# Performance work log

Measured on AMD Instinct MI355X. Metric: run time of the kernel, lower is better.

## Reference

```python
import jax, jax.numpy as jnp
import numpy as np

B, S, I, H, O, L = 16, 2048, 128, 512, 128, 2

def setup_inputs() -> dict:
    key = jax.random.key(0)
    ks = jax.random.split(key, 20)
    sI = 1.0 / np.sqrt(I)
    sH = 1.0 / np.sqrt(H)
    inp = {
        "x": jax.random.normal(ks[0], (B, S, I), jnp.float32),
        "hidden_state": jax.random.normal(ks[1], (B, L, H), jnp.float32),
        # layer 0 (input dim I)
        "Wxz0": jax.random.normal(ks[2], (H, I), jnp.float32) * sI,
        "Whz0": jax.random.normal(ks[3], (H, H), jnp.float32) * sH,
        "bhz0": jax.random.normal(ks[4], (H,), jnp.float32) * sH,
        "Wxr0": jax.random.normal(ks[5], (H, I), jnp.float32) * sI,
        "Whr0": jax.random.normal(ks[6], (H, H), jnp.float32) * sH,
        "bhr0": jax.random.normal(ks[7], (H,), jnp.float32) * sH,
        # layer 1 (input dim H)
        "Wxz1": jax.random.normal(ks[8], (H, H), jnp.float32) * sH,
        "Whz1": jax.random.normal(ks[9], (H, H), jnp.float32) * sH,
        "bhz1": jax.random.normal(ks[10], (H,), jnp.float32) * sH,
        "Wxr1": jax.random.normal(ks[11], (H, H), jnp.float32) * sH,
        "Whr1": jax.random.normal(ks[12], (H, H), jnp.float32) * sH,
        "bhr1": jax.random.normal(ks[13], (H,), jnp.float32) * sH,
        # output head
        "Why": jax.random.normal(ks[14], (O, H), jnp.float32) * sH,
        "by": jax.random.normal(ks[15], (O,), jnp.float32) * sH,
    }
    return inp


def _gru_layer(xs, h0, Wxz, Whz, bhz, Wxr, Whr, bhr):
    # Precompute input projections in one batched GEMM: [B,S,H]
    xz = jnp.einsum('bsi,hi->bsh', xs, Wxz)
    xr = jnp.einsum('bsi,hi->bsh', xs, Wxr)

    def step(h, inp):
        xz_t, xr_t = inp  # [B,H] each
        z = jax.nn.sigmoid(xz_t + h @ Whz.T + bhz)
        r = jax.nn.sigmoid(xr_t + h @ Whr.T + bhr)
        # NOTE: faithful to source bug: gt reuses fc_xr / fc_hr (with bias)
        g = jnp.tanh(xr_t + (r * h) @ Whr.T + bhr)
        hn = z * h + (1.0 - z) * g
        return hn, hn

    hT, ys = jax.lax.scan(step, h0, (jnp.swapaxes(xz, 0, 1), jnp.swapaxes(xr, 0, 1)))
    return jnp.swapaxes(ys, 0, 1), hT  # [B,S,H], [B,H]


def reference(x, hidden_state, Wxz0, Whz0, bhz0, Wxr0, Whr0, bhr0,
              Wxz1, Whz1, bhz1, Wxr1, Whr1, bhr1, Why, by):
    y0, h0T = _gru_layer(x, hidden_state[:, 0, :], Wxz0, Whz0, bhz0, Wxr0, Whr0, bhr0)
    y1, h1T = _gru_layer(y0, hidden_state[:, 1, :], Wxz1, Whz1, bhz1, Wxr1, Whr1, bhr1)
    out = jnp.einsum('bsh,oh->bso', y1, Why) + by  # [B,S,O]
    h_final = jnp.stack([h0T, h1T], axis=1)  # [B,L,H]
    return out, h_final
```

## Files before the change

kernel.cpp:

```cpp
#include <hip/hip_runtime.h>
#include <stdint.h>

#define Bv 16
#define Sv 2048
#define Iv 128
#define Hv 512
#define Ov 128
#define RP 520

typedef __bf16 v8bf __attribute__((ext_vector_type(8)));
typedef float v4f __attribute__((ext_vector_type(4)));
#define MFMA(a, b, c) __builtin_amdgcn_mfma_f32_16x16x32_bf16((a), (b), (c), 0, 0, 0)

__device__ __forceinline__ float sigf(float x) { return 1.0f / (1.0f + __expf(-x)); }
__device__ __forceinline__ float tanh_fast(float x) { return 2.0f / (1.0f + __expf(-2.0f * x)) - 1.0f; }

__device__ __forceinline__ unsigned f2bf(float f) {
  union { __bf16 h; unsigned short u; } c; c.h = (__bf16)f; return (unsigned)c.u;
}
__device__ __forceinline__ float bf2f(unsigned short u) {
  union { __bf16 h; unsigned short u; } c; c.u = u; return (float)c.h;
}

__device__ __forceinline__ v8bf cvt8(const float* p) {
  v8bf r;
#pragma unroll
  for (int i = 0; i < 8; i++) r[i] = (__bf16)p[i];
  return r;
}

__device__ __forceinline__ uint64_t ld64(const uint64_t* p) {
  return __hip_atomic_load((uint64_t*)p, __ATOMIC_RELAXED, __HIP_MEMORY_SCOPE_AGENT);
}
__device__ __forceinline__ void st32(unsigned* p, unsigned v) {
  __hip_atomic_store(p, v, __ATOMIC_RELAXED, __HIP_MEMORY_SCOPE_AGENT);
}
__device__ __forceinline__ unsigned ld32(const unsigned* p) {
  return __hip_atomic_load((unsigned*)p, __ATOMIC_RELAXED, __HIP_MEMORY_SCOPE_AGENT);
}

__device__ __forceinline__ void store_slice(unsigned* dslot, int rb, int j0, int rj, float val) {
  unsigned bits = f2bf(val);
  unsigned nb = (unsigned)__shfl_xor((int)bits, 1);
  if ((rj & 1) == 0)
    st32(dslot + rb * 256 + ((j0 + rj) >> 1), bits | (nb << 16));
}

__device__ __forceinline__ void poll1(const unsigned* s, unsigned want, int tid) {
  unsigned r = 0;
  for (;;) {
    unsigned v = ld32(s + (tid & 31));
    if (__all(v == want) || ++r > (1u << 20)) break;
  }
}
__device__ __forceinline__ void poll2(const unsigned* sA, unsigned wA,
                                      const unsigned* sB, unsigned wB, int tid) {
  unsigned r = 0;
  for (;;) {
    unsigned a = ld32(sA + (tid & 31));
    unsigned b = ld32(sB + (tid & 31));
    if (__all((a == wA) && (b == wB)) || ++r > (1u << 20)) break;
  }
}

__device__ __forceinline__ void read_stage(const unsigned* dslot, unsigned short* lds, int tid) {
  const uint64_t* p = (const uint64_t*)dslot;
  uint64_t w[8];
#pragma unroll
  for (int i = 0; i < 8; i++) w[i] = ld64(p + i * 256 + tid);
#pragma unroll
  for (int i = 0; i < 8; i++) {
    int d = i * 256 + tid;
    *(uint64_t*)(lds + (d >> 7) * RP + (d & 127) * 4) = w[i];
  }
}
__device__ __forceinline__ void read_stage2(const unsigned* dA, unsigned short* lA,
                                            const unsigned* dB, unsigned short* lB, int tid) {
  const uint64_t* pA = (const uint64_t*)dA;
  const uint64_t* pB = (const uint64_t*)dB;
  uint64_t wa[8], wb[8];
#pragma unroll
  for (int i = 0; i < 8; i++) wa[i] = ld64(pA + i * 256 + tid);
#pragma unroll
  for (int i = 0; i < 8; i++) wb[i] = ld64(pB + i * 256 + tid);
#pragma unroll
  for (int i = 0; i < 8; i++) {
    int d = i * 256 + tid;
    *(uint64_t*)(lA + (d >> 7) * RP + (d & 127) * 4) = wa[i];
    *(uint64_t*)(lB + (d >> 7) * RP + (d & 127) * 4) = wb[i];
  }
}

__global__ __launch_bounds__(256, 1) void gru_fused(
    const float* __restrict__ x, const float* __restrict__ hs,
    const float* __restrict__ Wxz0, const float* __restrict__ Whz0, const float* __restrict__ bhz0,
    const float* __restrict__ Wxr0, const float* __restrict__ Whr0, const float* __restrict__ bhr0,
    const float* __restrict__ Wxz1, const float* __restrict__ Whz1, const float* __restrict__ bhz1,
    const float* __restrict__ Wxr1, const float* __restrict__ Whr1, const float* __restrict__ bhr1,
    const float* __restrict__ Why, const float* __restrict__ by,
    float* __restrict__ out, char* __restrict__ ws, int D) {
  const int tid = threadIdx.x;
  const int wave = tid >> 6;
  const int lane = tid & 63;
  const int lm = lane & 15;
  const int lq = lane >> 4;
  const int rb = tid >> 4;
  const int rj = tid & 15;
  const int m0 = D - 1;

  unsigned* prog = (unsigned*)ws;
  unsigned* h0s = (unsigned*)(ws + 1024);
  unsigned* h1s = h0s + D * 32;
  unsigned* u0s = h1s + 128;
  unsigned* u1s = u0s + 64;
  unsigned* h0d = (unsigned*)(ws + 16384);
  unsigned* h1d = h0d + (size_t)D * 4096;
  unsigned* u0d = h1d + 4 * 4096;
  unsigned* u1d = u0d + 2 * 4096;

  __shared__ unsigned short stA[16 * RP];
  __shared__ unsigned short stB[16 * RP];
  __shared__ unsigned short stC[16 * RP];
  __shared__ float red[4][4][16][17];

  const bool L0 = (blockIdx.x < 32);
  const int wg = L0 ? blockIdx.x : (blockIdx.x - 32);
  const int j0 = wg << 4;
  const bool OW = (!L0) && (wg < 8);
  const int jrow = j0 + lm;

  {
    float h0v = hs[((size_t)rb * 2 + (L0 ? 0 : 1)) * Hv + j0 + rj];
    store_slice(L0 ? h0d : h1d, rb, j0, rj, h0v);
    __syncthreads();
    if (tid == 0) st32((L0 ? h0s : h1s) + wg, 1u);
  }

  if (L0) {
    v8bf wzx0 = cvt8(Wxz0 + (size_t)jrow * Iv + wave * 32 + lq * 8);
    v8bf wrx0 = cvt8(Wxr0 + (size_t)jrow * Iv + wave * 32 + lq * 8);
    v8bf wzh[4], wrh[4];
#pragma unroll
    for (int kb = 0; kb < 4; kb++) {
      int k = wave * 128 + kb * 32 + lq * 8;
      wzh[kb] = cvt8(Whz0 + (size_t)jrow * Hv + k);
      wrh[kb] = cvt8(Whr0 + (size_t)jrow * Hv + k);
    }
    float bz = bhz0[j0 + rj], br = bhr0[j0 + rj];

    const int xk = wave * 32 + lq * 8;
    float4 xp0 = *(const float4*)(x + ((size_t)lm * Sv + 0) * Iv + xk);
    float4 xp1 = *(const float4*)(x + ((size_t)lm * Sv + 0) * Iv + xk + 4);

    for (int t = 0; t < Sv; ++t) {
      if (t >= D - 1 && tid < 32) {
        unsigned need = (unsigned)(t - D + 2), it = 0;
        while (ld32(prog + tid) < need)
          if (++it > (1u << 20)) break;
      }
      poll1(h0s + (t & m0) * 32, (unsigned)(t + 1), tid);
      read_stage(h0d + (size_t)(t & m0) * 4096, stA, tid);
      __syncthreads();
      float hval = bf2f(stA[rb * RP + j0 + rj]);
      const unsigned short* hrow = stA + lm * RP;
      v8bf ah[4];
#pragma unroll
      for (int kb = 0; kb < 4; kb++)
        ah[kb] = *(const v8bf*)(hrow + wave * 128 + kb * 32 + lq * 8);
      v8bf ax;
      {
        float xf[8] = {xp0.x, xp0.y, xp0.z, xp0.w, xp1.x, xp1.y, xp1.z, xp1.w};
#pragma unroll
        for (int i = 0; i < 8; i++) ax[i] = (__bf16)xf[i];
      }
      v4f az = {0, 0, 0, 0}, axr = {0, 0, 0, 0}, ahr = {0, 0, 0, 0};
      az = MFMA(ax, wzx0, az);
      axr = MFMA(ax, wrx0, axr);
#pragma unroll
      for (int kb = 0; kb < 4; kb++) {
        az = MFMA(ah[kb], wzh[kb], az);
        ahr = MFMA(ah[kb], wrh[kb], ahr);
      }
#pragma unroll
      for (int v = 0; v < 4; v++) {
        red[0][wave][lq * 4 + v][lm] = az[v];
        red[1][wave][lq * 4 + v][lm] = axr[v];
        red[2][wave][lq * 4 + v][lm] = ahr[v];
      }
      __syncthreads();
      float zs = 0, xrs = 0, hrs = 0;
#pragma unroll
      for (int w = 0; w < 4; w++) {
        zs += red[0][w][rb][rj];
        xrs += red[1][w][rb][rj];
        hrs += red[2][w][rb][rj];
      }
      float z = sigf(zs + bz);
      float r = sigf(xrs + hrs + br);
      store_slice(u0d + (t & 1) * 4096, rb, j0, rj, r * hval);
      if (t + 1 < Sv) {
        xp0 = *(const float4*)(x + ((size_t)lm * Sv + (t + 1)) * Iv + xk);
        xp1 = *(const float4*)(x + ((size_t)lm * Sv + (t + 1)) * Iv + xk + 4);
      }
      __syncthreads();
      if (tid == 0) st32(u0s + (t & 1) * 32 + wg, (unsigned)(t + 1));
      poll1(u0s + (t & 1) * 32, (unsigned)(t + 1), tid);
      read_stage(u0d + (size_t)(t & 1) * 4096, stB, tid);
      __syncthreads();
      const unsigned short* urow = stB + lm * RP;
      v4f ag = {0, 0, 0, 0};
#pragma unroll
      for (int kb = 0; kb < 4; kb++) {
        v8bf au = *(const v8bf*)(urow + wave * 128 + kb * 32 + lq * 8);
        ag = MFMA(au, wrh[kb], ag);
      }
#pragma unroll
      for (int v = 0; v < 4; v++) red[3][wave][lq * 4 + v][lm] = ag[v];
      __syncthreads();
      float gs = 0;
#pragma unroll
      for (int w = 0; w < 4; w++) gs += red[3][w][rb][rj];
      float g = tanh_fast(xrs + gs + br);
      float hn = z * hval + (1.f - z) * g;
      store_slice(h0d + (size_t)((t + 1) & m0) * 4096, rb, j0, rj, hn);
      if (t == Sv - 1) out[(size_t)Bv * Sv * Ov + ((size_t)rb * 2 + 0) * Hv + j0 + rj] = hn;
      __syncthreads();
      if (tid == 0) st32(h0s + ((t + 1) & m0) * 32 + wg, (unsigned)(t + 2));
    }
  } else {
    v8bf wzx1[4], wrx1[4], wzh[4], wrh[4], wo[4];
#pragma unroll
    for (int kb = 0; kb < 4; kb++) {
      int k = wave * 128 + kb * 32 + lq * 8;
      wzx1[kb] = cvt8(Wxz1 + (size_t)jrow * Hv + k);
      wrx1[kb] = cvt8(Wxr1 + (size_t)jrow * Hv + k);
      wzh[kb] = cvt8(Whz1 + (size_t)jrow * Hv + k);
      wrh[kb] = cvt8(Whr1 + (size_t)jrow * Hv + k);
      if (OW) wo[kb] = cvt8(Why + (size_t)jrow * Hv + k);
    }
    float bz = bhz1[j0 + rj], br = bhr1[j0 + rj];
    float bo = OW ? by[j0 + rj] : 0.f;

    for (int t = 0; t < Sv; ++t) {
      poll2(h0s + ((t + 1) & m0) * 32, (unsigned)(t + 2),
            h1s + (t & 3) * 32, (unsigned)(t + 1), tid);
      read_stage2(h0d + (size_t)((t + 1) & m0) * 4096, stA,
                  h1d + (size_t)(t & 3) * 4096, stB, tid);
      __syncthreads();
      if (tid == 0) st32(prog + wg, (unsigned)(t + 1));
      float hval = bf2f(stB[rb * RP + j0 + rj]);
      const unsigned short* yrow = stA + lm * RP;
      const unsigned short* hrow = stB + lm * RP;
      v4f az = {0, 0, 0, 0}, axr = {0, 0, 0, 0}, ahr = {0, 0, 0, 0}, ao = {0, 0, 0, 0};
      v8bf ahf[4];
#pragma unroll
      for (int kb = 0; kb < 4; kb++) {
        int k = wave * 128 + kb * 32 + lq * 8;
        v8bf ay = *(const v8bf*)(yrow + k);
        ahf[kb] = *(const v8bf*)(hrow + k);
        az = MFMA(ay, wzx1[kb], az);
        az = MFMA(ahf[kb], wzh[kb], az);
        axr = MFMA(ay, wrx1[kb], axr);
        ahr = MFMA(ahf[kb], wrh[kb], ahr);
      }
      if (OW && t > 0) {
#pragma unroll
        for (int kb = 0; kb < 4; kb++) ao = MFMA(ahf[kb], wo[kb], ao);
      }
#pragma unroll
      for (int v = 0; v < 4; v++) {
        red[0][wave][lq * 4 + v][lm] = az[v];
        red[1][wave][lq * 4 + v][lm] = axr[v];
        red[2][wave][lq * 4 + v][lm] = ahr[v];
        red[3][wave][lq * 4 + v][lm] = ao[v];
      }
      __syncthreads();
      float zs = 0, xrs = 0, hrs = 0, os = 0;
#pragma unroll
      for (int w = 0; w < 4; w++) {
        zs += red[0][w][rb][rj];
        xrs += red[1][w][rb][rj];
        hrs += red[2][w][rb][rj];
        os += red[3][w][rb][rj];
      }
      float z = sigf(zs + bz);
      float r = sigf(xrs + hrs + br);
      store_slice(u1d + (t & 1) * 4096, rb, j0, rj, r * hval);
      if (OW && t > 0) out[((size_t)rb * Sv + (t - 1)) * Ov + j0 + rj] = os + bo;
      __syncthreads();
      if (tid == 0) st32(u1s + (t & 1) * 32 + wg, (unsigned)(t + 1));
      poll1(u1s + (t & 1) * 32, (unsigned)(t + 1), tid);
      read_stage(u1d + (size_t)(t & 1) * 4096, stC, tid);
      __syncthreads();
      const unsigned short* urow = stC + lm * RP;
      v4f ag = {0, 0, 0, 0};
#pragma unroll
      for (int kb = 0; kb < 4; kb++) {
        v8bf au = *(const v8bf*)(urow + wave * 128 + kb * 32 + lq * 8);
        ag = MFMA(au, wrh[kb], ag);
      }
#pragma unroll
      for (int v = 0; v < 4; v++) red[3][wave][lq * 4 + v][lm] = ag[v];
      __syncthreads();
      float gs = 0;
#pragma unroll
      for (int w = 0; w < 4; w++) gs += red[3][w][rb][rj];
      float g = tanh_fast(xrs + gs + br);
      float hn = z * hval + (1.f - z) * g;
      store_slice(h1d + (size_t)((t + 1) & 3) * 4096, rb, j0, rj, hn);
      if (t == Sv - 1) out[(size_t)Bv * Sv * Ov + ((size_t)rb * 2 + 1) * Hv + j0 + rj] = hn;
      __syncthreads();
      if (tid == 0) st32(h1s + ((t + 1) & 3) * 32 + wg, (unsigned)(t + 2));
    }
    if (OW) {
      poll1(h1s + (Sv & 3) * 32, (unsigned)(Sv + 1), tid);
      read_stage(h1d + (size_t)(Sv & 3) * 4096, stB, tid);
      __syncthreads();
      const unsigned short* hrow = stB + lm * RP;
      v4f ao = {0, 0, 0, 0};
#pragma unroll
      for (int kb = 0; kb < 4; kb++) {
        v8bf ah = *(const v8bf*)(hrow + wave * 128 + kb * 32 + lq * 8);
        ao = MFMA(ah, wo[kb], ao);
      }
#pragma unroll
      for (int v = 0; v < 4; v++) red[3][wave][lq * 4 + v][lm] = ao[v];
      __syncthreads();
      float os = 0;
#pragma unroll
      for (int w = 0; w < 4; w++) os += red[3][w][rb][rj];
      out[((size_t)rb * Sv + (Sv - 1)) * Ov + j0 + rj] = os + bo;
    }
  }
}

extern "C" void kernel_launch(void* const* d_in, const int* in_sizes, int n_in,
                              void* d_out, int out_size, void* d_ws, size_t ws_size,
                              hipStream_t stream) {
  const float* x = (const float*)d_in[0];
  const float* hs = (const float*)d_in[1];
  const float* Wxz0 = (const float*)d_in[2];
  const float* Whz0 = (const float*)d_in[3];
  const float* bhz0 = (const float*)d_in[4];
  const float* Wxr0 = (const float*)d_in[5];
  const float* Whr0 = (const float*)d_in[6];
  const float* bhr0 = (const float*)d_in[7];
  const float* Wxz1 = (const float*)d_in[8];
  const float* Whz1 = (const float*)d_in[9];
  const float* bhz1 = (const float*)d_in[10];
  const float* Wxr1 = (const float*)d_in[11];
  const float* Whr1 = (const float*)d_in[12];
  const float* bhr1 = (const float*)d_in[13];
  const float* Why = (const float*)d_in[14];
  const float* by = (const float*)d_in[15];
  float* out = (float*)d_out;

  int D = 64;
  while (D > 4 && 16384 + (size_t)(D + 8) * 16384 > ws_size) D >>= 1;

  hipMemsetAsync(d_ws, 0, 4096, stream);
  hipLaunchKernelGGL(gru_fused, dim3(64), dim3(256), 0, stream,
                     x, hs, Wxz0, Whz0, bhz0, Wxr0, Whr0, bhr0,
                     Wxz1, Whz1, bhz1, Wxr1, Whr1, bhr1, Why, by,
                     out, (char*)d_ws, D);
}
```

Measured before the change: 9.004 ms.

## Replace flag-based cross-block sync with tagged per-element data and fragment-layout polling

Each bf16 hidden-state element is now stored in a 32-bit word together with a timestep tag. Data sits in a permuted layout matching the MFMA fragment order, so each lane polls and loads its own operands straight from global memory. This removes the separate flag arrays, the LDS staging buffers, the __syncthreads around stores and the flag publish/poll round trip, trading one fence-like handshake per stage for doubled workspace traffic and per-lane validation loops. It also moves the prefetch and progress wait earlier, adds a separate reduction slot for the g-gate, and memsets the whole workspace each call.

Result: slower. 25.53 ms (+183.5%).

```diff
diff --git a/kernel.cpp b/kernel.cpp
--- a/kernel.cpp
+++ b/kernel.cpp
@@ -6,7 +6,6 @@
 #define Iv 128
 #define Hv 512
 #define Ov 128
-#define RP 520
 
 typedef __bf16 v8bf __attribute__((ext_vector_type(8)));
 typedef float v4f __attribute__((ext_vector_type(4)));
@@ -39,55 +38,79 @@
   return __hip_atomic_load((unsigned*)p, __ATOMIC_RELAXED, __HIP_MEMORY_SCOPE_AGENT);
 }
 
-__device__ __forceinline__ void store_slice(unsigned* dslot, int rb, int j0, int rj, float val) {
-  unsigned bits = f2bf(val);
-  unsigned nb = (unsigned)__shfl_xor((int)bits, 1);
-  if ((rj & 1) == 0)
-    st32(dslot + rb * 256 + ((j0 + rj) >> 1), bits | (nb << 16));
-}
-
-__device__ __forceinline__ void poll1(const unsigned* s, unsigned want, int tid) {
+__device__ __forceinline__ int pidx(int b, int c) {
+  return ((c >> 7) << 11) | (((c >> 3) & 3) << 9) | (b << 5) | (((c >> 5) & 3) << 3) | (c & 7);
+}
+
+__device__ __forceinline__ void pollfrag(const unsigned* slot, int wl, unsigned tag, uint64_t* W) {
+  const uint64_t* p = (const uint64_t*)slot + wl;
+  const uint64_t want = ((uint64_t)tag << 16) | ((uint64_t)tag << 48);
+  const uint64_t MSK = 0xffff0000ffff0000ull;
   unsigned r = 0;
   for (;;) {
-    unsigned v = ld32(s + (tid & 31));
-    if (__all(v == want) || ++r > (1u << 20)) break;
+    uint64_t a0 = ld64(p), a1 = ld64(p + 4), a2 = ld64(p + 8), a3 = ld64(p + 12);
+    bool probe = ((a0 & MSK) == want) && ((a1 & MSK) == want) &&
+                 ((a2 & MSK) == want) && ((a3 & MSK) == want);
+    if (__all(probe)) {
+#pragma unroll
+      for (int i = 0; i < 16; i++) W[i] = ld64(p + i);
+      bool ok = true;
+#pragma unroll
+      for (int i = 0; i < 16; i++) ok &= ((W[i] & MSK) == want);
+      if (__all(ok)) return;
+    }
+    if (++r > (1u << 20)) {
+#pragma unroll
+      for (int i = 0; i < 16; i++) W[i] = ld64(p + i);
+      return;
+    }
   }
 }
-__device__ __forceinline__ void poll2(const unsigned* sA, unsigned wA,
-                                      const unsigned* sB, unsigned wB, int tid) {
+
+__device__ __forceinline__ void pollfrag2(const unsigned* sA, unsigned tA,
+                                          const unsigned* sB, unsigned tB,
+                                          int wl, uint64_t* WA, uint64_t* WB) {
+  const uint64_t* pA = (const uint64_t*)sA + wl;
+  const uint64_t* pB = (const uint64_t*)sB + wl;
+  const uint64_t wantA = ((uint64_t)tA << 16) | ((uint64_t)tA << 48);
+  const uint64_t wantB = ((uint64_t)tB << 16) | ((uint64_t)tB << 48);
+  const uint64_t MSK = 0xffff0000ffff0000ull;
   unsigned r = 0;
   for (;;) {
-    unsigned a = ld32(sA + (tid & 31));
-    unsigned b = ld32(sB + (tid & 31));
-    if (__all((a == wA) && (b == wB)) || ++r > (1u << 20)) break;
+    uint64_t a0 = ld64(pA), a1 = ld64(pA + 4), a2 = ld64(pA + 8), a3 = ld64(pA + 12);
+    uint64_t b0 = ld64(pB), b1 = ld64(pB + 4), b2 = ld64(pB + 8), b3 = ld64(pB + 12);
+    bool probe = ((a0 & MSK) == wantA) && ((a1 & MSK) == wantA) &&
+                 ((a2 & MSK) == wantA) && ((a3 & MSK) == wantA) &&
+                 ((b0 & MSK) == wantB) && ((b1 & MSK) == wantB) &&
+                 ((b2 & MSK) == wantB) && ((b3 & MSK) == wantB);
+    if (__all(probe)) {
+#pragma unroll
+      for (int i = 0; i < 16; i++) WA[i] = ld64(pA + i);
+#pragma unroll
+      for (int i = 0; i < 16; i++) WB[i] = ld64(pB + i);
+      bool ok = true;
+#pragma unroll
+      for (int i = 0; i < 16; i++) ok &= ((WA[i] & MSK) == wantA) & ((WB[i] & MSK) == wantB);
+      if (__all(ok)) return;
+    }
+    if (++r > (1u << 20)) {
+#pragma unroll
+      for (int i = 0; i < 16; i++) { WA[i] = ld64(pA + i); WB[i] = ld64(pB + i); }
+      return;
+    }
   }
 }
 
-__device__ __forceinline__ void read_stage(const unsigned* dslot, unsigned short* lds, int tid) {
-  const uint64_t* p = (const uint64_t*)dslot;
-  uint64_t w[8];
-#pragma unroll
-  for (int i = 0; i < 8; i++) w[i] = ld64(p + i * 256 + tid);
-#pragma unroll
-  for (int i = 0; i < 8; i++) {
-    int d = i * 256 + tid;
-    *(uint64_t*)(lds + (d >> 7) * RP + (d & 127) * 4) = w[i];
-  }
-}
-__device__ __forceinline__ void read_stage2(const unsigned* dA, unsigned short* lA,
-                                            const unsigned* dB, unsigned short* lB, int tid) {
-  const uint64_t* pA = (const uint64_t*)dA;
-  const uint64_t* pB = (const uint64_t*)dB;
-  uint64_t wa[8], wb[8];
-#pragma unroll
-  for (int i = 0; i < 8; i++) wa[i] = ld64(pA + i * 256 + tid);
-#pragma unroll
-  for (int i = 0; i < 8; i++) wb[i] = ld64(pB + i * 256 + tid);
-#pragma unroll
-  for (int i = 0; i < 8; i++) {
-    int d = i * 256 + tid;
-    *(uint64_t*)(lA + (d >> 7) * RP + (d & 127) * 4) = wa[i];
-    *(uint64_t*)(lB + (d >> 7) * RP + (d & 127) * 4) = wb[i];
+__device__ __forceinline__ void mkfrags(const uint64_t* W, v8bf* ah) {
+#pragma unroll
+  for (int kb = 0; kb < 4; kb++) {
+    union { v8bf v; uint32_t q[4]; } cc;
+#pragma unroll
+    for (int j = 0; j < 4; j++) {
+      uint64_t w = W[kb * 4 + j];
+      cc.q[j] = (uint32_t)(w & 0xffffu) | (((uint32_t)(w >> 32)) << 16);
+    }
+    ah[kb] = cc.v;
   }
 }
 
@@ -106,22 +129,16 @@
   const int lq = lane >> 4;
   const int rb = tid >> 4;
   const int rj = tid & 15;
+  const int wl = wave * 1024 + lane * 16;
   const int m0 = D - 1;
 
   unsigned* prog = (unsigned*)ws;
-  unsigned* h0s = (unsigned*)(ws + 1024);
-  unsigned* h1s = h0s + D * 32;
-  unsigned* u0s = h1s + 128;
-  unsigned* u1s = u0s + 64;
   unsigned* h0d = (unsigned*)(ws + 16384);
-  unsigned* h1d = h0d + (size_t)D * 4096;
-  unsigned* u0d = h1d + 4 * 4096;
-  unsigned* u1d = u0d + 2 * 4096;
-
-  __shared__ unsigned short stA[16 * RP];
-  __shared__ unsigned short stB[16 * RP];
-  __shared__ unsigned short stC[16 * RP];
-  __shared__ float red[4][4][16][17];
+  unsigned* h1d = h0d + (size_t)D * 8192;
+  unsigned* u0d = h1d + 4 * 8192;
+  unsigned* u1d = u0d + 2 * 8192;
+
+  __shared__ float red[5][4][16][17];
 
   const bool L0 = (blockIdx.x < 32);
   const int wg = L0 ? blockIdx.x : (blockIdx.x - 32);
@@ -129,16 +146,10 @@
   const bool OW = (!L0) && (wg < 8);
   const int jrow = j0 + lm;
 
-  {
-    float h0v = hs[((size_t)rb * 2 + (L0 ? 0 : 1)) * Hv + j0 + rj];
-    store_slice(L0 ? h0d : h1d, rb, j0, rj, h0v);
-    __syncthreads();
-    if (tid == 0) st32((L0 ? h0s : h1s) + wg, 1u);
-  }
-
   if (L0) {
-    v8bf wzx0 = cvt8(Wxz0 + (size_t)jrow * Iv + wave * 32 + lq * 8);
-    v8bf wrx0 = cvt8(Wxr0 + (size_t)jrow * Iv + wave * 32 + lq * 8);
+    const int xk = wave * 32 + lq * 8;
+    v8bf wzx0 = cvt8(Wxz0 + (size_t)jrow * Iv + xk);
+    v8bf wrx0 = cvt8(Wxr0 + (size_t)jrow * Iv + xk);
     v8bf wzh[4], wrh[4];
 #pragma unroll
     for (int kb = 0; kb < 4; kb++) {
@@ -148,25 +159,16 @@
     }
     float bz = bhz0[j0 + rj], br = bhr0[j0 + rj];
 
-    const int xk = wave * 32 + lq * 8;
+    float hval = bf2f((unsigned short)f2bf(hs[((size_t)rb * 2 + 0) * Hv + j0 + rj]));
+    st32(h0d + pidx(rb, j0 + rj), f2bf(hval) | (1u << 16));
+
     float4 xp0 = *(const float4*)(x + ((size_t)lm * Sv + 0) * Iv + xk);
     float4 xp1 = *(const float4*)(x + ((size_t)lm * Sv + 0) * Iv + xk + 4);
 
     for (int t = 0; t < Sv; ++t) {
-      if (t >= D - 1 && tid < 32) {
-        unsigned need = (unsigned)(t - D + 2), it = 0;
-        while (ld32(prog + tid) < need)
-          if (++it > (1u << 20)) break;
-      }
-      poll1(h0s + (t & m0) * 32, (unsigned)(t + 1), tid);
-      read_stage(h0d + (size_t)(t & m0) * 4096, stA, tid);
-      __syncthreads();
-      float hval = bf2f(stA[rb * RP + j0 + rj]);
-      const unsigned short* hrow = stA + lm * RP;
-      v8bf ah[4];
-#pragma unroll
-      for (int kb = 0; kb < 4; kb++)
-        ah[kb] = *(const v8bf*)(hrow + wave * 128 + kb * 32 + lq * 8);
+      uint64_t W[16];
+      pollfrag(h0d + (size_t)(t & m0) * 8192, wl, (unsigned)(t + 1), W);
+      v8bf ah[4]; mkfrags(W, ah);
       v8bf ax;
       {
         float xf[8] = {xp0.x, xp0.y, xp0.z, xp0.w, xp1.x, xp1.y, xp1.z, xp1.w};
@@ -187,6 +189,15 @@
         red[1][wave][lq * 4 + v][lm] = axr[v];
         red[2][wave][lq * 4 + v][lm] = ahr[v];
       }
+      if (t + 1 < Sv) {
+        xp0 = *(const float4*)(x + ((size_t)lm * Sv + (t + 1)) * Iv + xk);
+        xp1 = *(const float4*)(x + ((size_t)lm * Sv + (t + 1)) * Iv + xk + 4);
+      }
+      if (t >= D - 1) {
+        unsigned need = (unsigned)(t - D + 2), it = 0;
+        while (ld32(prog + (tid & 31)) < need)
+          if (++it > (1u << 20)) break;
+      }
       __syncthreads();
       float zs = 0, xrs = 0, hrs = 0;
 #pragma unroll
@@ -197,35 +208,28 @@
       }
       float z = sigf(zs + bz);
       float r = sigf(xrs + hrs + br);
-      store_slice(u0d + (t & 1) * 4096, rb, j0, rj, r * hval);
-      if (t + 1 < Sv) {
-        xp0 = *(const float4*)(x + ((size_t)lm * Sv + (t + 1)) * Iv + xk);
-        xp1 = *(const float4*)(x + ((size_t)lm * Sv + (t + 1)) * Iv + xk + 4);
-      }
-      __syncthreads();
-      if (tid == 0) st32(u0s + (t & 1) * 32 + wg, (unsigned)(t + 1));
-      poll1(u0s + (t & 1) * 32, (unsigned)(t + 1), tid);
-      read_stage(u0d + (size_t)(t & 1) * 4096, stB, tid);
-      __syncthreads();
-      const unsigned short* urow = stB + lm * RP;
+      st32(u0d + (size_t)(t & 1) * 8192 + pidx(rb, j0 + rj),
+           f2bf(r * hval) | ((unsigned)(t + 1) << 16));
+      uint64_t WU[16];
+      pollfrag(u0d + (size_t)(t & 1) * 8192, wl, (unsigned)(t + 1), WU);
+      v8bf au[4]; mkfrags(WU, au);
       v4f ag = {0, 0, 0, 0};
 #pragma unroll
-      for (int kb = 0; kb < 4; kb++) {
-        v8bf au = *(const v8bf*)(urow + wave * 128 + kb * 32 + lq * 8);
-        ag = MFMA(au, wrh[kb], ag);
-      }
-#pragma unroll
-      for (int v = 0; v < 4; v++) red[3][wave][lq * 4 + v][lm] = ag[v];
+      for (int kb = 0; kb < 4; kb++) ag = MFMA(au[kb], wrh[kb], ag);
+#pragma unroll
+      for (int v = 0; v < 4; v++) red[4][wave][lq * 4 + v][lm] = ag[v];
       __syncthreads();
       float gs = 0;
 #pragma unroll
-      for (int w = 0; w < 4; w++) gs += red[3][w][rb][rj];
+      for (int w = 0; w < 4; w++) gs += red[4][w][rb][rj];
       float g = tanh_fast(xrs + gs + br);
       float hn = z * hval + (1.f - z) * g;
-      store_slice(h0d + (size_t)((t + 1) & m0) * 4096, rb, j0, rj, hn);
-      if (t == Sv - 1) out[(size_t)Bv * Sv * Ov + ((size_t)rb * 2 + 0) * Hv + j0 + rj] = hn;
-      __syncthreads();
-      if (tid == 0) st32(h0s + ((t + 1) & m0) * 32 + wg, (unsigned)(t + 2));
+      unsigned hb = f2bf(hn);
+      hval = bf2f((unsigned short)hb);
+      st32(h0d + (size_t)((t + 1) & m0) * 8192 + pidx(rb, j0 + rj),
+           hb | ((unsigned)(t + 2) << 16));
+      if (t == Sv - 1)
+        out[(size_t)Bv * Sv * Ov + ((size_t)rb * 2 + 0) * Hv + j0 + rj] = hn;
     }
   } else {
     v8bf wzx1[4], wrx1[4], wzh[4], wrh[4], wo[4];
@@ -241,26 +245,22 @@
     float bz = bhz1[j0 + rj], br = bhr1[j0 + rj];
     float bo = OW ? by[j0 + rj] : 0.f;
 
+    float hval = bf2f((unsigned short)f2bf(hs[((size_t)rb * 2 + 1) * Hv + j0 + rj]));
+    st32(h1d + pidx(rb, j0 + rj), f2bf(hval) | (1u << 16));
+
     for (int t = 0; t < Sv; ++t) {
-      poll2(h0s + ((t + 1) & m0) * 32, (unsigned)(t + 2),
-            h1s + (t & 3) * 32, (unsigned)(t + 1), tid);
-      read_stage2(h0d + (size_t)((t + 1) & m0) * 4096, stA,
-                  h1d + (size_t)(t & 3) * 4096, stB, tid);
-      __syncthreads();
-      if (tid == 0) st32(prog + wg, (unsigned)(t + 1));
-      float hval = bf2f(stB[rb * RP + j0 + rj]);
-      const unsigned short* yrow = stA + lm * RP;
-      const unsigned short* hrow = stB + lm * RP;
+      uint64_t WY[16], WH[16];
+      pollfrag2(h0d + (size_t)((t + 1) & m0) * 8192, (unsigned)(t + 2),
+                h1d + (size_t)(t & 3) * 8192, (unsigned)(t + 1), wl, WY, WH);
+      v8bf ay[4], ahf[4];
+      mkfrags(WY, ay);
+      mkfrags(WH, ahf);
       v4f az = {0, 0, 0, 0}, axr = {0, 0, 0, 0}, ahr = {0, 0, 0, 0}, ao = {0, 0, 0, 0};
-      v8bf ahf[4];
 #pragma unroll
       for (int kb = 0; kb < 4; kb++) {
-        int k = wave * 128 + kb * 32 + lq * 8;
-        v8bf ay = *(const v8bf*)(yrow + k);
-        ahf[kb] = *(const v8bf*)(hrow + k);
-        az = MFMA(ay, wzx1[kb], az);
+        az = MFMA(ay[kb], wzx1[kb], az);
         az = MFMA(ahf[kb], wzh[kb], az);
-        axr = MFMA(ay, wrx1[kb], axr);
+        axr = MFMA(ay[kb], wrx1[kb], axr);
         ahr = MFMA(ahf[kb], wrh[kb], ahr);
       }
       if (OW && t > 0) {
@@ -272,57 +272,51 @@
         red[0][wave][lq * 4 + v][lm] = az[v];
         red[1][wave][lq * 4 + v][lm] = axr[v];
         red[2][wave][lq * 4 + v][lm] = ahr[v];
-        red[3][wave][lq * 4 + v][lm] = ao[v];
-      }
-      __syncthreads();
+        if (OW) red[3][wave][lq * 4 + v][lm] = ao[v];
+      }
+      __syncthreads();
+      if (tid == 0) st32(prog + wg, (unsigned)(t + 1));
       float zs = 0, xrs = 0, hrs = 0, os = 0;
 #pragma unroll
       for (int w = 0; w < 4; w++) {
         zs += red[0][w][rb][rj];
         xrs += red[1][w][rb][rj];
         hrs += red[2][w][rb][rj];
-        os += red[3][w][rb][rj];
+        if (OW) os += red[3][w][rb][rj];
       }
       float z = sigf(zs + bz);
       float r = sigf(xrs + hrs + br);
-      store_slice(u1d + (t & 1) * 4096, rb, j0, rj, r * hval);
+      st32(u1d + (size_t)(t & 1) * 8192 + pidx(rb, j0 + rj),
+           f2bf(r * hval) | ((unsigned)(t + 1) << 16));
       if (OW && t > 0) out[((size_t)rb * Sv + (t - 1)) * Ov + j0 + rj] = os + bo;
-      __syncthreads();
-      if (tid == 0) st32(u1s + (t & 1) * 32 + wg, (unsigned)(t + 1));
-      poll1(u1s + (t & 1) * 32, (unsigned)(t + 1), tid);
-      read_stage(u1d + (size_t)(t & 1) * 4096, stC, tid);
-      __syncthreads();
-      const unsigned short* urow = stC + lm * RP;
+      uint64_t WU[16];
+      pollfrag(u1d + (size_t)(t & 1) * 8192, wl, (unsigned)(t + 1), WU);
+      v8bf au[4]; mkfrags(WU, au);
       v4f ag = {0, 0, 0, 0};
 #pragma unroll
-      for (int kb = 0; kb < 4; kb++) {
-        v8bf au = *(const v8bf*)(urow + wave * 128 + kb * 32 + lq * 8);
-        ag = MFMA(au, wrh[kb], ag);
-      }
-#pragma unroll
-      for (int v = 0; v < 4; v++) red[3][wave][lq * 4 + v][lm] = ag[v];
+      for (int kb = 0; kb < 4; kb++) ag = MFMA(au[kb], wrh[kb], ag);
+#pragma unroll
+      for (int v = 0; v < 4; v++) red[4][wave][lq * 4 + v][lm] = ag[v];
       __syncthreads();
       float gs = 0;
 #pragma unroll
-      for (int w = 0; w < 4; w++) gs += red[3][w][rb][rj];
+      for (int w = 0; w < 4; w++) gs += red[4][w][rb][rj];
       float g = tanh_fast(xrs + gs + br);
       float hn = z * hval + (1.f - z) * g;
-      store_slice(h1d + (size_t)((t + 1) & 3) * 4096, rb, j0, rj, hn);
-      if (t == Sv - 1) out[(size_t)Bv * Sv * Ov + ((size_t)rb * 2 + 1) * Hv + j0 + rj] = hn;
-      __syncthreads();
-      if (tid == 0) st32(h1s + ((t + 1) & 3) * 32 + wg, (unsigned)(t + 2));
+      unsigned hb = f2bf(hn);
+      hval = bf2f((unsigned short)hb);
+      st32(h1d + (size_t)((t + 1) & 3) * 8192 + pidx(rb, j0 + rj),
+           hb | ((unsigned)(t + 2) << 16));
+      if (t == Sv - 1)
+        out[(size_t)Bv * Sv * Ov + ((size_t)rb * 2 + 1) * Hv + j0 + rj] = hn;
     }
     if (OW) {
-      poll1(h1s + (Sv & 3) * 32, (unsigned)(Sv + 1), tid);
-      read_stage(h1d + (size_t)(Sv & 3) * 4096, stB, tid);
-      __syncthreads();
-      const unsigned short* hrow = stB + lm * RP;
+      uint64_t W[16];
+      pollfrag(h1d + (size_t)(Sv & 3) * 8192, wl, (unsigned)(Sv + 1), W);
+      v8bf ah[4]; mkfrags(W, ah);
       v4f ao = {0, 0, 0, 0};
 #pragma unroll
-      for (int kb = 0; kb < 4; kb++) {
-        v8bf ah = *(const v8bf*)(hrow + wave * 128 + kb * 32 + lq * 8);
-        ao = MFMA(ah, wo[kb], ao);
-      }
+      for (int kb = 0; kb < 4; kb++) ao = MFMA(ah[kb], wo[kb], ao);
 #pragma unroll
       for (int v = 0; v < 4; v++) red[3][wave][lq * 4 + v][lm] = ao[v];
       __syncthreads();
@@ -356,9 +350,11 @@
   float* out = (float*)d_out;
 
   int D = 64;
-  while (D > 4 && 16384 + (size_t)(D + 8) * 16384 > ws_size) D >>= 1;
-
-  hipMemsetAsync(d_ws, 0, 4096, stream);
+  while (D > 4 && 16384 + (size_t)(D + 8) * 32768 > ws_size) D >>= 1;
+
+  size_t msz = 16384 + (size_t)(D + 8) * 32768;
+  if (msz > ws_size) msz = ws_size;
+  hipMemsetAsync(d_ws, 0, msz, stream);
   hipLaunchKernelGGL(gru_fused, dim3(64), dim3(256), 0, stream,
                      x, hs, Wxz0, Whz0, bhz0, Wxr0, Whr0, bhr0,
                      Wxz1, Whz1, bhz1, Wxr1, Whr1, bhr1, Why, by,
```

## Use LDS-only barriers and move flow-control polls off the recurrent critical path

Applied to the files above, without the earlier changes.

Swaps the __syncthreads calls that guard LDS traffic for a barrier that waits only on lgkmcnt, so the next x prefetch and other outstanding global loads no longer stall the barrier. Layer 0's backpressure poll on layer-1 progress moves from the start of each step to just before the hidden-state publish. The gate reduction gets its own red slot, which removes a write-after-read hazard on the shared buffer, and the output store moves after the step's flag publish. The risk is subtle: the inline-asm barrier could miss other pending memory ops, and the wider memset suggests the workspace layout assumptions changed.

Result: slower. 9.329 ms (+3.6%).

```diff
diff --git a/kernel.cpp b/kernel.cpp
--- a/kernel.cpp
+++ b/kernel.cpp
@@ -27,6 +27,10 @@
 #pragma unroll
   for (int i = 0; i < 8; i++) r[i] = (__bf16)p[i];
   return r;
+}
+
+__device__ __forceinline__ void lgkm_barrier() {
+  asm volatile("s_waitcnt lgkmcnt(0)\n\ts_barrier" ::: "memory");
 }
 
 __device__ __forceinline__ uint64_t ld64(const uint64_t* p) {
@@ -121,7 +125,7 @@
   __shared__ unsigned short stA[16 * RP];
   __shared__ unsigned short stB[16 * RP];
   __shared__ unsigned short stC[16 * RP];
-  __shared__ float red[4][4][16][17];
+  __shared__ float red[5][4][16][17];
 
   const bool L0 = (blockIdx.x < 32);
   const int wg = L0 ? blockIdx.x : (blockIdx.x - 32);
@@ -153,26 +157,25 @@
     float4 xp1 = *(const float4*)(x + ((size_t)lm * Sv + 0) * Iv + xk + 4);
 
     for (int t = 0; t < Sv; ++t) {
-      if (t >= D - 1 && tid < 32) {
-        unsigned need = (unsigned)(t - D + 2), it = 0;
-        while (ld32(prog + tid) < need)
-          if (++it > (1u << 20)) break;
-      }
       poll1(h0s + (t & m0) * 32, (unsigned)(t + 1), tid);
       read_stage(h0d + (size_t)(t & m0) * 4096, stA, tid);
-      __syncthreads();
+      v8bf ax;
+      {
+        float xf[8] = {xp0.x, xp0.y, xp0.z, xp0.w, xp1.x, xp1.y, xp1.z, xp1.w};
+#pragma unroll
+        for (int i = 0; i < 8; i++) ax[i] = (__bf16)xf[i];
+      }
+      if (t + 1 < Sv) {
+        xp0 = *(const float4*)(x + ((size_t)lm * Sv + (t + 1)) * Iv + xk);
+        xp1 = *(const float4*)(x + ((size_t)lm * Sv + (t + 1)) * Iv + xk + 4);
+      }
+      lgkm_barrier();
       float hval = bf2f(stA[rb * RP + j0 + rj]);
       const unsigned short* hrow = stA + lm * RP;
       v8bf ah[4];
 #pragma unroll
       for (int kb = 0; kb < 4; kb++)
         ah[kb] = *(const v8bf*)(hrow + wave * 128 + kb * 32 + lq * 8);
-      v8bf ax;
-      {
-        float xf[8] = {xp0.x, xp0.y, xp0.z, xp0.w, xp1.x, xp1.y, xp1.z, xp1.w};
-#pragma unroll
-        for (int i = 0; i < 8; i++) ax[i] = (__bf16)xf[i];
-      }
       v4f az = {0, 0, 0, 0}, axr = {0, 0, 0, 0}, ahr = {0, 0, 0, 0};
       az = MFMA(ax, wzx0, az);
       axr = MFMA(ax, wrx0, axr);
@@ -187,7 +190,7 @@
         red[1][wave][lq * 4 + v][lm] = axr[v];
         red[2][wave][lq * 4 + v][lm] = ahr[v];
       }
-      __syncthreads();
+      lgkm_barrier();
       float zs = 0, xrs = 0, hrs = 0;
 #pragma unroll
       for (int w = 0; w < 4; w++) {
@@ -197,16 +200,12 @@
       }
       float z = sigf(zs + bz);
       float r = sigf(xrs + hrs + br);
-      store_slice(u0d + (t & 1) * 4096, rb, j0, rj, r * hval);
-      if (t + 1 < Sv) {
-        xp0 = *(const float4*)(x + ((size_t)lm * Sv + (t + 1)) * Iv + xk);
-        xp1 = *(const float4*)(x + ((size_t)lm * Sv + (t + 1)) * Iv + xk + 4);
-      }
+      store_slice(u0d + (size_t)(t & 1) * 4096, rb, j0, rj, r * hval);
       __syncthreads();
       if (tid == 0) st32(u0s + (t & 1) * 32 + wg, (unsigned)(t + 1));
       poll1(u0s + (t & 1) * 32, (unsigned)(t + 1), tid);
       read_stage(u0d + (size_t)(t & 1) * 4096, stB, tid);
-      __syncthreads();
+      lgkm_barrier();
       const unsigned short* urow = stB + lm * RP;
       v4f ag = {0, 0, 0, 0};
 #pragma unroll
@@ -215,13 +214,18 @@
         ag = MFMA(au, wrh[kb], ag);
       }
 #pragma unroll
-      for (int v = 0; v < 4; v++) red[3][wave][lq * 4 + v][lm] = ag[v];
-      __syncthreads();
+      for (int v = 0; v < 4; v++) red[4][wave][lq * 4 + v][lm] = ag[v];
+      lgkm_barrier();
       float gs = 0;
 #pragma unroll
-      for (int w = 0; w < 4; w++) gs += red[3][w][rb][rj];
+      for (int w = 0; w < 4; w++) gs += red[4][w][rb][rj];
       float g = tanh_fast(xrs + gs + br);
       float hn = z * hval + (1.f - z) * g;
+      if (t >= D - 1) {
+        unsigned need = (unsigned)(t - D + 2), it = 0;
+        while (ld32(prog + (tid & 31)) < need)
+          if (++it > (1u << 20)) break;
+      }
       store_slice(h0d + (size_t)((t + 1) & m0) * 4096, rb, j0, rj, hn);
       if (t == Sv - 1) out[(size_t)Bv * Sv * Ov + ((size_t)rb * 2 + 0) * Hv + j0 + rj] = hn;
       __syncthreads();
@@ -246,7 +250,7 @@
             h1s + (t & 3) * 32, (unsigned)(t + 1), tid);
       read_stage2(h0d + (size_t)((t + 1) & m0) * 4096, stA,
                   h1d + (size_t)(t & 3) * 4096, stB, tid);
-      __syncthreads();
+      lgkm_barrier();
       if (tid == 0) st32(prog + wg, (unsigned)(t + 1));
       float hval = bf2f(stB[rb * RP + j0 + rj]);
       const unsigned short* yrow = stA + lm * RP;
@@ -272,26 +276,25 @@
         red[0][wave][lq * 4 + v][lm] = az[v];
         red[1][wave][lq * 4 + v][lm] = axr[v];
         red[2][wave][lq * 4 + v][lm] = ahr[v];
-        red[3][wave][lq * 4 + v][lm] = ao[v];
-      }
-      __syncthreads();
+        if (OW) red[3][wave][lq * 4 + v][lm] = ao[v];
+      }
+      lgkm_barrier();
       float zs = 0, xrs = 0, hrs = 0, os = 0;
 #pragma unroll
       for (int w = 0; w < 4; w++) {
         zs += red[0][w][rb][rj];
         xrs += red[1][w][rb][rj];
         hrs += red[2][w][rb][rj];
-        os += red[3][w][rb][rj];
+        if (OW) os += red[3][w][rb][rj];
       }
       float z = sigf(zs + bz);
       float r = sigf(xrs + hrs + br);
-      store_slice(u1d + (t & 1) * 4096, rb, j0, rj, r * hval);
-      if (OW && t > 0) out[((size_t)rb * Sv + (t - 1)) * Ov + j0 + rj] = os + bo;
+      store_slice(u1d + (size_t)(t & 1) * 4096, rb, j0, rj, r * hval);
       __syncthreads();
       if (tid == 0) st32(u1s + (t & 1) * 32 + wg, (unsigned)(t + 1));
       poll1(u1s + (t & 1) * 32, (unsigned)(t + 1), tid);
       read_stage(u1d + (size_t)(t & 1) * 4096, stC, tid);
-      __syncthreads();
+      lgkm_barrier();
       const unsigned short* urow = stC + lm * RP;
       v4f ag = {0, 0, 0, 0};
 #pragma unroll
@@ -300,17 +303,18 @@
         ag = MFMA(au, wrh[kb], ag);
       }
 #pragma unroll
-      for (int v = 0; v < 4; v++) red[3][wave][lq * 4 + v][lm] = ag[v];
-      __syncthreads();
+      for (int v = 0; v < 4; v++) red[4][wave][lq * 4 + v][lm] = ag[v];
+      lgkm_barrier();
       float gs = 0;
 #pragma unroll
-      for (int w = 0; w < 4; w++) gs += red[3][w][rb][rj];
+      for (int w = 0; w < 4; w++) gs += red[4][w][rb][rj];
       float g = tanh_fast(xrs + gs + br);
       float hn = z * hval + (1.f - z) * g;
       store_slice(h1d + (size_t)((t + 1) & 3) * 4096, rb, j0, rj, hn);
       if (t == Sv - 1) out[(size_t)Bv * Sv * Ov + ((size_t)rb * 2 + 1) * Hv + j0 + rj] = hn;
       __syncthreads();
       if (tid == 0) st32(h1s + ((t + 1) & 3) * 32 + wg, (unsigned)(t + 2));
+      if (OW && t > 0) out[((size_t)rb * Sv + (t - 1)) * Ov + j0 + rj] = os + bo;
     }
     if (OW) {
       poll1(h1s + (Sv & 3) * 32, (unsigned)(Sv + 1), tid);
@@ -358,7 +362,7 @@
   int D = 64;
   while (D > 4 && 16384 + (size_t)(D + 8) * 16384 > ws_size) D >>= 1;
 
-  hipMemsetAsync(d_ws, 0, 4096, stream);
+  hipMemsetAsync(d_ws, 0, 12288, stream);
   hipLaunchKernelGGL(gru_fused, dim3(64), dim3(256), 0, stream,
                      x, hs, Wxz0, Whz0, bhz0, Wxr0, Whr0, bhr0,
                      Wxz1, Whz1, bhz1, Wxr1, Whr1, bhr1, Why, by,
```
